# Performance work log

Hardware: AMD Instinct MI355X
Metric: run time of the kernel (lower is better)

Reference implementation:

```python
import jax, jax.numpy as jnp
import numpy as np

NUM_ROUNDS = 3


def squash(x, axis=-1):
    # s_norm / (1 + s_norm) * x / sqrt(s_norm), matching the torch code exactly
    s_norm = jnp.sum(x * x, axis=axis, keepdims=True)
    return (s_norm / (1.0 + s_norm)) * x / jnp.sqrt(s_norm)


def setup_inputs() -> dict:
    key = jax.random.key(0)
    k1, k2 = jax.random.split(key)
    x = jax.random.normal(k1, (512, 1152, 8), dtype=jnp.float32)   # [B, R, Cin]
    W = jax.random.normal(k2, (10, 1152, 8, 16), dtype=jnp.float32)  # [N, R, Cin, Cout]
    return {"x": x, "W": W}


def reference(x, W):
    # priors = x[None,:,:,None,:] @ W[:,None,:,:,:]  -> [N, B, R, 1, Cout]
    priors = jnp.einsum('bri,nrio->nbro', x, W)[:, :, :, None, :]
    logits = jnp.zeros_like(priors)  # [N, B, R, 1, Cout]
    outps = None
    for i in range(NUM_ROUNDS):
        probs = jax.nn.softmax(logits, axis=2)  # softmax over routes R
        outps = squash(jnp.sum(probs * priors, axis=2, keepdims=True))  # [N, B, 1, 1, Cout]
        if i != NUM_ROUNDS - 1:
            # agreement logit update: dot over Cout
            logits = logits + jnp.sum(priors * outps, axis=-1, keepdims=True)
    return outps
```

## Files before the change

kernel.cpp:

```cpp
#include <hip/hip_runtime.h>
#include <math.h>

#define R_ROUTES 1152
#define CIN 8
#define COUT 16
#define BATCH 512
#define NCAPS 10
#define NUM_ROUNDS 3

typedef __fp16 h2 __attribute__((ext_vector_type(2)));
union U32H2 { unsigned int u; h2 h; };

__device__ __forceinline__ unsigned int pkrtz(float lo, float hi) {
    U32H2 v; v.h = __builtin_amdgcn_cvt_pkrtz(lo, hi);
    return v.u;
}
__device__ __forceinline__ h2 as_h2(unsigned int u) { U32H2 v; v.u = u; return v.h; }
__device__ __forceinline__ float f_lo(unsigned int u) { return (float)as_h2(u).x; }
__device__ __forceinline__ float f_hi(unsigned int u) { return (float)as_h2(u).y; }
__device__ __forceinline__ float dot2(unsigned int p, unsigned int s, float c) {
    return __builtin_amdgcn_fdot2(as_h2(p), as_h2(s), c, false);
}

__device__ __forceinline__ int sunit(int r, int h) {
    return (2 * r + h) ^ ((r >> 2) & 7);
}

extern "C" __global__ void __launch_bounds__(256)
pack_w(const float* __restrict__ W, unsigned int* __restrict__ Wp)
{
    const int tau = blockIdx.x * 256 + threadIdx.x;
    const int o = tau & 15;
    const int nr = tau >> 4;
    const float* __restrict__ src = W + (size_t)nr * 128 + o;
    uint4 u;
    u.x = pkrtz(src[0],  src[16]);
    u.y = pkrtz(src[32], src[48]);
    u.z = pkrtz(src[64], src[80]);
    u.w = pkrtz(src[96], src[112]);
    *(uint4*)(Wp + (size_t)tau * 4) = u;
}

extern "C" __global__ void __launch_bounds__(512, 4)
capsule_routing_v9(const float* __restrict__ x,
                   const unsigned int* __restrict__ Wp,
                   float* __restrict__ out)
{
    __shared__ unsigned int pbuf[2 * R_ROUTES * 8];
    __shared__ float wred[16 * 16];
    __shared__ float red[2 * 32 * 20];
    __shared__ float sred[2 * 4];
    __shared__ float sv[2 * 16];

    const int blk = blockIdx.x;
    const int n = blk >> 8;
    const int bp = blk & 255;
    const int t = threadIdx.x;

    const float* __restrict__ x0 = x + (size_t)(2 * bp) * (R_ROUTES * CIN);
    const float* __restrict__ x1 = x0 + R_ROUTES * CIN;
    const unsigned int* __restrict__ Wn = Wp + (size_t)n * (R_ROUTES * 64);

    float cs[2][4] = {{0.f, 0.f, 0.f, 0.f}, {0.f, 0.f, 0.f, 0.f}};
    {
        const int q = t >> 2;
        const int oq = t & 3;
        const int subw = (oq & 1) * 2;
        const int hq = oq >> 1;

        #pragma unroll 1
        for (int it = 0; it < 9; ++it) {
            const int r = it * 128 + q;
            const unsigned int* __restrict__ wb = Wn + (size_t)r * 64;
            const uint4 w0 = *(const uint4*)(wb + (oq + 0) * 4);
            const uint4 w1 = *(const uint4*)(wb + (oq + 4) * 4);
            const uint4 w2 = *(const uint4*)(wb + (oq + 8) * 4);
            const uint4 w3 = *(const uint4*)(wb + (oq + 12) * 4);
            const float4 xa0 = *(const float4*)(x0 + r * 8);
            const float4 xa1 = *(const float4*)(x0 + r * 8 + 4);
            const float4 xb0 = *(const float4*)(x1 + r * 8);
            const float4 xb1 = *(const float4*)(x1 + r * 8 + 4);

            {
                const unsigned int xp0 = pkrtz(xa0.x, xa0.y), xp1 = pkrtz(xa0.z, xa0.w);
                const unsigned int xp2 = pkrtz(xa1.x, xa1.y), xp3 = pkrtz(xa1.z, xa1.w);
                const float p0 = dot2(w0.w, xp3, dot2(w0.z, xp2, dot2(w0.y, xp1, dot2(w0.x, xp0, 0.f))));
                const float p1 = dot2(w1.w, xp3, dot2(w1.z, xp2, dot2(w1.y, xp1, dot2(w1.x, xp0, 0.f))));
                const float p2 = dot2(w2.w, xp3, dot2(w2.z, xp2, dot2(w2.y, xp1, dot2(w2.x, xp0, 0.f))));
                const float p3 = dot2(w3.w, xp3, dot2(w3.z, xp2, dot2(w3.y, xp1, dot2(w3.x, xp0, 0.f))));
                cs[0][0] += p0; cs[0][1] += p1; cs[0][2] += p2; cs[0][3] += p3;
                uint2 u; u.x = pkrtz(p0, p1); u.y = pkrtz(p2, p3);
                *(uint2*)(pbuf + sunit(r, hq) * 4 + subw) = u;
            }
            {
                const unsigned int xp0 = pkrtz(xb0.x, xb0.y), xp1 = pkrtz(xb0.z, xb0.w);
                const unsigned int xp2 = pkrtz(xb1.x, xb1.y), xp3 = pkrtz(xb1.z, xb1.w);
                const float p0 = dot2(w0.w, xp3, dot2(w0.z, xp2, dot2(w0.y, xp1, dot2(w0.x, xp0, 0.f))));
                const float p1 = dot2(w1.w, xp3, dot2(w1.z, xp2, dot2(w1.y, xp1, dot2(w1.x, xp0, 0.f))));
                const float p2 = dot2(w2.w, xp3, dot2(w2.z, xp2, dot2(w2.y, xp1, dot2(w2.x, xp0, 0.f))));
                const float p3 = dot2(w3.w, xp3, dot2(w3.z, xp2, dot2(w3.y, xp1, dot2(w3.x, xp0, 0.f))));
                cs[1][0] += p0; cs[1][1] += p1; cs[1][2] += p2; cs[1][3] += p3;
                uint2 u; u.x = pkrtz(p0, p1); u.y = pkrtz(p2, p3);
                *(uint2*)(pbuf + R_ROUTES * 8 + sunit(r, hq) * 4 + subw) = u;
            }
        }

        #pragma unroll
        for (int mask = 4; mask <= 32; mask <<= 1) {
            #pragma unroll
            for (int b = 0; b < 2; ++b)
                #pragma unroll
                for (int j = 0; j < 4; ++j)
                    cs[b][j] += __shfl_xor(cs[b][j], mask, 64);
        }
        if ((t & 63) < 4) {
            const int w = t >> 6;
            *(float4*)(wred + (w * 2 + 0) * 16 + 4 * oq) =
                make_float4(cs[0][0], cs[0][1], cs[0][2], cs[0][3]);
            *(float4*)(wred + (w * 2 + 1) * 16 + 4 * oq) =
                make_float4(cs[1][0], cs[1][1], cs[1][2], cs[1][3]);
        }
    }
    __syncthreads();

    const int half = t >> 8;
    const int tt = t & 255;
    unsigned int* __restrict__ pb = pbuf + half * (R_ROUTES * 8);
    float* __restrict__ redh = red + half * (32 * 20);
    float* __restrict__ sredh = sred + half * 4;
    float* __restrict__ svh = sv + half * 16;

    if (tt < 16) {
        float s = 0.f;
        #pragma unroll
        for (int w = 0; w < 8; ++w) s += wred[(w * 2 + half) * 16 + tt];
        svh[tt] = s * (1.0f / (float)R_ROUTES);
    }
    __syncthreads();

    float sn = 0.f;
    #pragma unroll
    for (int o = 0; o < 16; ++o) { const float s = svh[o]; sn = fmaf(s, s, sn); }
    float factor = sn / ((1.0f + sn) * sqrtf(sn));

    const int nr = (tt < 128) ? 5 : 4;
    float bl[5] = {0.f, 0.f, 0.f, 0.f, 0.f};

    #pragma unroll 1
    for (int pass = 1; pass < NUM_ROUNDS; ++pass) {
        unsigned int svp[8];
        #pragma unroll
        for (int s = 0; s < 8; ++s)
            svp[s] = pkrtz(svh[2 * s], svh[2 * s + 1]);
        float acc[16];
        #pragma unroll
        for (int o = 0; o < 16; ++o) acc[o] = 0.f;
        float es = 0.f;

        #pragma unroll
        for (int k = 0; k < 5; ++k) {
            if (k < nr) {
                const int r = tt + (k << 8);
                const uint4 a = *(const uint4*)(pb + sunit(r, 0) * 4);
                const uint4 c = *(const uint4*)(pb + sunit(r, 1) * 4);
                float d = 0.f;
                d = dot2(a.x, svp[0], d);
                d = dot2(a.y, svp[1], d);
                d = dot2(a.z, svp[2], d);
                d = dot2(a.w, svp[3], d);
                d = dot2(c.x, svp[4], d);
                d = dot2(c.y, svp[5], d);
                d = dot2(c.z, svp[6], d);
                d = dot2(c.w, svp[7], d);
                bl[k] = fmaf(factor, d, bl[k]);
                const float e = __expf(bl[k]);
                es += e;
                acc[0]  = fmaf(e, f_lo(a.x), acc[0]);
                acc[1]  = fmaf(e, f_hi(a.x), acc[1]);
                acc[2]  = fmaf(e, f_lo(a.y), acc[2]);
                acc[3]  = fmaf(e, f_hi(a.y), acc[3]);
                acc[4]  = fmaf(e, f_lo(a.z), acc[4]);
                acc[5]  = fmaf(e, f_hi(a.z), acc[5]);
                acc[6]  = fmaf(e, f_lo(a.w), acc[6]);
                acc[7]  = fmaf(e, f_hi(a.w), acc[7]);
                acc[8]  = fmaf(e, f_lo(c.x), acc[8]);
                acc[9]  = fmaf(e, f_hi(c.x), acc[9]);
                acc[10] = fmaf(e, f_lo(c.y), acc[10]);
                acc[11] = fmaf(e, f_hi(c.y), acc[11]);
                acc[12] = fmaf(e, f_lo(c.z), acc[12]);
                acc[13] = fmaf(e, f_hi(c.z), acc[13]);
                acc[14] = fmaf(e, f_lo(c.w), acc[14]);
                acc[15] = fmaf(e, f_hi(c.w), acc[15]);
            }
        }
        #pragma unroll
        for (int off = 32; off > 0; off >>= 1) es += __shfl_xor(es, off, 64);
        if ((t & 63) == 0) sredh[tt >> 6] = es;

        #pragma unroll
        for (int o = 0; o < 16; ++o) {
            acc[o] += __shfl_xor(acc[o], 1, 64);
            acc[o] += __shfl_xor(acc[o], 2, 64);
            acc[o] += __shfl_xor(acc[o], 4, 64);
        }
        if ((tt & 7) == 0) {
            float* dst = redh + (tt >> 3) * 20;
            *(float4*)(dst + 0)  = make_float4(acc[0],  acc[1],  acc[2],  acc[3]);
            *(float4*)(dst + 4)  = make_float4(acc[4],  acc[5],  acc[6],  acc[7]);
            *(float4*)(dst + 8)  = make_float4(acc[8],  acc[9],  acc[10], acc[11]);
            *(float4*)(dst + 12) = make_float4(acc[12], acc[13], acc[14], acc[15]);
        }
        __syncthreads();

        if (tt < 16) {
            float s = 0.f;
            #pragma unroll
            for (int w = 0; w < 32; ++w) s += redh[w * 20 + tt];
            const float Z = sredh[0] + sredh[1] + sredh[2] + sredh[3];
            svh[tt] = s / Z;
        }
        __syncthreads();

        sn = 0.f;
        #pragma unroll
        for (int o = 0; o < 16; ++o) { const float s = svh[o]; sn = fmaf(s, s, sn); }
        factor = sn / ((1.0f + sn) * sqrtf(sn));
    }

    if (tt < 16) {
        const int o = (tt >> 2) + ((tt & 3) << 2);
        out[((size_t)n * BATCH + 2 * bp + half) * COUT + o] = factor * svh[tt];
    }
}

extern "C" void kernel_launch(void* const* d_in, const int* in_sizes, int n_in,
                              void* d_out, int out_size, void* d_ws, size_t ws_size,
                              hipStream_t stream) {
    const float* x = (const float*)d_in[0];
    const float* W = (const float*)d_in[1];
    float* out = (float*)d_out;
    unsigned int* Wp = (unsigned int*)d_ws;

    pack_w<<<dim3(NCAPS * R_ROUTES * COUT / 256), dim3(256), 0, stream>>>(W, Wp);
    capsule_routing_v9<<<dim3(NCAPS * (BATCH / 2)), dim3(512), 0, stream>>>(x, Wp, out);
}
```

Measured before the change: 136.4 us.

## Pre-pack x to fp16 in prep kernel and software-pipeline routing loads

Extends the weight-packing kernel to also convert x to packed fp16, so the routing kernel reads half as many bytes of x for each of the ten capsules and skips the per-block conversion. The first routing loop is double-buffered across iterations so the loads for the next route chunk are issued before the current chunk's dot products. A fallback path keeps the old behaviour when the workspace is too small. This costs an extra pass over x in the prep kernel and more registers in the main kernel.

After: 136.8 us. About the same (+0.3%).

```diff
diff --git a/kernel.cpp b/kernel.cpp
--- a/kernel.cpp
+++ b/kernel.cpp
@@ -8,6 +8,10 @@
 #define NCAPS 10
 #define NUM_ROUNDS 3
 
+#define WP_U32S (NCAPS * R_ROUTES * COUT * 4)
+#define XP_U32S (BATCH * R_ROUTES * 4)
+#define WS_NEED ((size_t)(WP_U32S + XP_U32S) * 4)
+
 typedef __fp16 h2 __attribute__((ext_vector_type(2)));
 union U32H2 { unsigned int u; h2 h; };
 
@@ -27,24 +31,71 @@
 }
 
 extern "C" __global__ void __launch_bounds__(256)
-pack_w(const float* __restrict__ W, unsigned int* __restrict__ Wp)
+pack_wx(const float* __restrict__ W, const float* __restrict__ x,
+        unsigned int* __restrict__ Wp, unsigned int* __restrict__ xp)
 {
-    const int tau = blockIdx.x * 256 + threadIdx.x;
-    const int o = tau & 15;
-    const int nr = tau >> 4;
-    const float* __restrict__ src = W + (size_t)nr * 128 + o;
-    uint4 u;
-    u.x = pkrtz(src[0],  src[16]);
-    u.y = pkrtz(src[32], src[48]);
-    u.z = pkrtz(src[64], src[80]);
-    u.w = pkrtz(src[96], src[112]);
-    *(uint4*)(Wp + (size_t)tau * 4) = u;
-}
+    const int bid = blockIdx.x;
+    if (bid < NCAPS * R_ROUTES * COUT / 256) {
+        const int tau = bid * 256 + threadIdx.x;
+        const int o = tau & 15;
+        const int nr = tau >> 4;
+        const float* __restrict__ src = W + (size_t)nr * 128 + o;
+        uint4 u;
+        u.x = pkrtz(src[0],  src[16]);
+        u.y = pkrtz(src[32], src[48]);
+        u.z = pkrtz(src[64], src[80]);
+        u.w = pkrtz(src[96], src[112]);
+        *(uint4*)(Wp + (size_t)tau * 4) = u;
+    } else {
+        const int idx = (bid - NCAPS * R_ROUTES * COUT / 256) * 256 + threadIdx.x;
+        const float4 v0 = *(const float4*)(x + (size_t)idx * 8);
+        const float4 v1 = *(const float4*)(x + (size_t)idx * 8 + 4);
+        uint4 u;
+        u.x = pkrtz(v0.x, v0.y); u.y = pkrtz(v0.z, v0.w);
+        u.z = pkrtz(v1.x, v1.y); u.w = pkrtz(v1.z, v1.w);
+        *(uint4*)(xp + (size_t)idx * 4) = u;
+    }
+}
+
+#define LOADS(IT, W0, W1, W2, W3, XA, XB)                                  \
+    {                                                                      \
+        const int r_ = (IT) * 128 + q;                                     \
+        const unsigned int* __restrict__ wb_ = Wn + (size_t)r_ * 64 + oq * 4; \
+        W0 = *(const uint4*)(wb_);                                         \
+        W1 = *(const uint4*)(wb_ + 16);                                    \
+        W2 = *(const uint4*)(wb_ + 32);                                    \
+        W3 = *(const uint4*)(wb_ + 48);                                    \
+        XA = *(const uint4*)(xp0 + (size_t)r_ * 4);                        \
+        XB = *(const uint4*)(xp1 + (size_t)r_ * 4);                        \
+    }
+
+#define COMPUTES(IT, W0, W1, W2, W3, XA, XB)                               \
+    {                                                                      \
+        const int r_ = (IT) * 128 + q;                                     \
+        {                                                                  \
+            const float p0 = dot2(W0.w, XA.w, dot2(W0.z, XA.z, dot2(W0.y, XA.y, dot2(W0.x, XA.x, 0.f)))); \
+            const float p1 = dot2(W1.w, XA.w, dot2(W1.z, XA.z, dot2(W1.y, XA.y, dot2(W1.x, XA.x, 0.f)))); \
+            const float p2 = dot2(W2.w, XA.w, dot2(W2.z, XA.z, dot2(W2.y, XA.y, dot2(W2.x, XA.x, 0.f)))); \
+            const float p3 = dot2(W3.w, XA.w, dot2(W3.z, XA.z, dot2(W3.y, XA.y, dot2(W3.x, XA.x, 0.f)))); \
+            cs00 += p0; cs01 += p1; cs02 += p2; cs03 += p3;                \
+            uint2 u_; u_.x = pkrtz(p0, p1); u_.y = pkrtz(p2, p3);          \
+            *(uint2*)(pbuf + sunit(r_, hq) * 4 + subw) = u_;               \
+        }                                                                  \
+        {                                                                  \
+            const float p0 = dot2(W0.w, XB.w, dot2(W0.z, XB.z, dot2(W0.y, XB.y, dot2(W0.x, XB.x, 0.f)))); \
+            const float p1 = dot2(W1.w, XB.w, dot2(W1.z, XB.z, dot2(W1.y, XB.y, dot2(W1.x, XB.x, 0.f)))); \
+            const float p2 = dot2(W2.w, XB.w, dot2(W2.z, XB.z, dot2(W2.y, XB.y, dot2(W2.x, XB.x, 0.f)))); \
+            const float p3 = dot2(W3.w, XB.w, dot2(W3.z, XB.z, dot2(W3.y, XB.y, dot2(W3.x, XB.x, 0.f)))); \
+            cs10 += p0; cs11 += p1; cs12 += p2; cs13 += p3;                \
+            uint2 u_; u_.x = pkrtz(p0, p1); u_.y = pkrtz(p2, p3);          \
+            *(uint2*)(pbuf + R_ROUTES * 8 + sunit(r_, hq) * 4 + subw) = u_; \
+        }                                                                  \
+    }
 
 extern "C" __global__ void __launch_bounds__(512, 4)
-capsule_routing_v9(const float* __restrict__ x,
-                   const unsigned int* __restrict__ Wp,
-                   float* __restrict__ out)
+capsule_routing_v10(const unsigned int* __restrict__ xp,
+                    const unsigned int* __restrict__ Wp,
+                    float* __restrict__ out)
 {
     __shared__ unsigned int pbuf[2 * R_ROUTES * 8];
     __shared__ float wred[16 * 16];
@@ -57,68 +108,42 @@
     const int bp = blk & 255;
     const int t = threadIdx.x;
 
-    const float* __restrict__ x0 = x + (size_t)(2 * bp) * (R_ROUTES * CIN);
-    const float* __restrict__ x1 = x0 + R_ROUTES * CIN;
+    const unsigned int* __restrict__ xp0 = xp + (size_t)(2 * bp) * (R_ROUTES * 4);
+    const unsigned int* __restrict__ xp1 = xp0 + R_ROUTES * 4;
     const unsigned int* __restrict__ Wn = Wp + (size_t)n * (R_ROUTES * 64);
 
-    float cs[2][4] = {{0.f, 0.f, 0.f, 0.f}, {0.f, 0.f, 0.f, 0.f}};
+    float cs00 = 0.f, cs01 = 0.f, cs02 = 0.f, cs03 = 0.f;
+    float cs10 = 0.f, cs11 = 0.f, cs12 = 0.f, cs13 = 0.f;
     {
         const int q = t >> 2;
         const int oq = t & 3;
         const int subw = (oq & 1) * 2;
         const int hq = oq >> 1;
 
+        uint4 wA0, wA1, wA2, wA3, xAa, xAb;
+        uint4 wB0, wB1, wB2, wB3, xBa, xBb;
+
+        LOADS(0, wA0, wA1, wA2, wA3, xAa, xAb);
         #pragma unroll 1
-        for (int it = 0; it < 9; ++it) {
-            const int r = it * 128 + q;
-            const unsigned int* __restrict__ wb = Wn + (size_t)r * 64;
-            const uint4 w0 = *(const uint4*)(wb + (oq + 0) * 4);
-            const uint4 w1 = *(const uint4*)(wb + (oq + 4) * 4);
-            const uint4 w2 = *(const uint4*)(wb + (oq + 8) * 4);
-            const uint4 w3 = *(const uint4*)(wb + (oq + 12) * 4);
-            const float4 xa0 = *(const float4*)(x0 + r * 8);
-            const float4 xa1 = *(const float4*)(x0 + r * 8 + 4);
-            const float4 xb0 = *(const float4*)(x1 + r * 8);
-            const float4 xb1 = *(const float4*)(x1 + r * 8 + 4);
-
-            {
-                const unsigned int xp0 = pkrtz(xa0.x, xa0.y), xp1 = pkrtz(xa0.z, xa0.w);
-                const unsigned int xp2 = pkrtz(xa1.x, xa1.y), xp3 = pkrtz(xa1.z, xa1.w);
-                const float p0 = dot2(w0.w, xp3, dot2(w0.z, xp2, dot2(w0.y, xp1, dot2(w0.x, xp0, 0.f))));
-                const float p1 = dot2(w1.w, xp3, dot2(w1.z, xp2, dot2(w1.y, xp1, dot2(w1.x, xp0, 0.f))));
-                const float p2 = dot2(w2.w, xp3, dot2(w2.z, xp2, dot2(w2.y, xp1, dot2(w2.x, xp0, 0.f))));
-                const float p3 = dot2(w3.w, xp3, dot2(w3.z, xp2, dot2(w3.y, xp1, dot2(w3.x, xp0, 0.f))));
-                cs[0][0] += p0; cs[0][1] += p1; cs[0][2] += p2; cs[0][3] += p3;
-                uint2 u; u.x = pkrtz(p0, p1); u.y = pkrtz(p2, p3);
-                *(uint2*)(pbuf + sunit(r, hq) * 4 + subw) = u;
-            }
-            {
-                const unsigned int xp0 = pkrtz(xb0.x, xb0.y), xp1 = pkrtz(xb0.z, xb0.w);
-                const unsigned int xp2 = pkrtz(xb1.x, xb1.y), xp3 = pkrtz(xb1.z, xb1.w);
-                const float p0 = dot2(w0.w, xp3, dot2(w0.z, xp2, dot2(w0.y, xp1, dot2(w0.x, xp0, 0.f))));
-                const float p1 = dot2(w1.w, xp3, dot2(w1.z, xp2, dot2(w1.y, xp1, dot2(w1.x, xp0, 0.f))));
-                const float p2 = dot2(w2.w, xp3, dot2(w2.z, xp2, dot2(w2.y, xp1, dot2(w2.x, xp0, 0.f))));
-                const float p3 = dot2(w3.w, xp3, dot2(w3.z, xp2, dot2(w3.y, xp1, dot2(w3.x, xp0, 0.f))));
-                cs[1][0] += p0; cs[1][1] += p1; cs[1][2] += p2; cs[1][3] += p3;
-                uint2 u; u.x = pkrtz(p0, p1); u.y = pkrtz(p2, p3);
-                *(uint2*)(pbuf + R_ROUTES * 8 + sunit(r, hq) * 4 + subw) = u;
-            }
-        }
+        for (int it = 0; it < 8; it += 2) {
+            LOADS(it + 1, wB0, wB1, wB2, wB3, xBa, xBb);
+            COMPUTES(it, wA0, wA1, wA2, wA3, xAa, xAb);
+            LOADS(it + 2, wA0, wA1, wA2, wA3, xAa, xAb);
+            COMPUTES(it + 1, wB0, wB1, wB2, wB3, xBa, xBb);
+        }
+        COMPUTES(8, wA0, wA1, wA2, wA3, xAa, xAb);
 
         #pragma unroll
         for (int mask = 4; mask <= 32; mask <<= 1) {
-            #pragma unroll
-            for (int b = 0; b < 2; ++b)
-                #pragma unroll
-                for (int j = 0; j < 4; ++j)
-                    cs[b][j] += __shfl_xor(cs[b][j], mask, 64);
+            cs00 += __shfl_xor(cs00, mask, 64); cs01 += __shfl_xor(cs01, mask, 64);
+            cs02 += __shfl_xor(cs02, mask, 64); cs03 += __shfl_xor(cs03, mask, 64);
+            cs10 += __shfl_xor(cs10, mask, 64); cs11 += __shfl_xor(cs11, mask, 64);
+            cs12 += __shfl_xor(cs12, mask, 64); cs13 += __shfl_xor(cs13, mask, 64);
         }
         if ((t & 63) < 4) {
             const int w = t >> 6;
-            *(float4*)(wred + (w * 2 + 0) * 16 + 4 * oq) =
-                make_float4(cs[0][0], cs[0][1], cs[0][2], cs[0][3]);
-            *(float4*)(wred + (w * 2 + 1) * 16 + 4 * oq) =
-                make_float4(cs[1][0], cs[1][1], cs[1][2], cs[1][3]);
+            *(float4*)(wred + (w * 2 + 0) * 16 + 4 * oq) = make_float4(cs00, cs01, cs02, cs03);
+            *(float4*)(wred + (w * 2 + 1) * 16 + 4 * oq) = make_float4(cs10, cs11, cs12, cs13);
         }
     }
     __syncthreads();
@@ -233,6 +258,192 @@
     }
 }
 
+extern "C" __global__ void __launch_bounds__(256)
+pack_w_only(const float* __restrict__ W, unsigned int* __restrict__ Wp)
+{
+    const int tau = blockIdx.x * 256 + threadIdx.x;
+    const int o = tau & 15;
+    const int nr = tau >> 4;
+    const float* __restrict__ src = W + (size_t)nr * 128 + o;
+    uint4 u;
+    u.x = pkrtz(src[0],  src[16]);
+    u.y = pkrtz(src[32], src[48]);
+    u.z = pkrtz(src[64], src[80]);
+    u.w = pkrtz(src[96], src[112]);
+    *(uint4*)(Wp + (size_t)tau * 4) = u;
+}
+
+extern "C" __global__ void __launch_bounds__(512, 4)
+capsule_routing_v9f(const float* __restrict__ x,
+                    const unsigned int* __restrict__ Wp,
+                    float* __restrict__ out)
+{
+    __shared__ unsigned int pbuf[2 * R_ROUTES * 8];
+    __shared__ float wred[16 * 16];
+    __shared__ float red[2 * 32 * 20];
+    __shared__ float sred[2 * 4];
+    __shared__ float sv[2 * 16];
+
+    const int blk = blockIdx.x;
+    const int n = blk >> 8;
+    const int bp = blk & 255;
+    const int t = threadIdx.x;
+
+    const float* __restrict__ x0 = x + (size_t)(2 * bp) * (R_ROUTES * CIN);
+    const float* __restrict__ x1 = x0 + R_ROUTES * CIN;
+    const unsigned int* __restrict__ Wn = Wp + (size_t)n * (R_ROUTES * 64);
+
+    float cs00 = 0.f, cs01 = 0.f, cs02 = 0.f, cs03 = 0.f;
+    float cs10 = 0.f, cs11 = 0.f, cs12 = 0.f, cs13 = 0.f;
+    {
+        const int q = t >> 2;
+        const int oq = t & 3;
+        const int subw = (oq & 1) * 2;
+        const int hq = oq >> 1;
+
+        #pragma unroll 1
+        for (int it = 0; it < 9; ++it) {
+            const int r = it * 128 + q;
+            const unsigned int* __restrict__ wb = Wn + (size_t)r * 64 + oq * 4;
+            const uint4 w0 = *(const uint4*)(wb);
+            const uint4 w1 = *(const uint4*)(wb + 16);
+            const uint4 w2 = *(const uint4*)(wb + 32);
+            const uint4 w3 = *(const uint4*)(wb + 48);
+            const float4 xa0 = *(const float4*)(x0 + r * 8);
+            const float4 xa1 = *(const float4*)(x0 + r * 8 + 4);
+            const float4 xb0 = *(const float4*)(x1 + r * 8);
+            const float4 xb1 = *(const float4*)(x1 + r * 8 + 4);
+            {
+                const unsigned int xq0 = pkrtz(xa0.x, xa0.y), xq1 = pkrtz(xa0.z, xa0.w);
+                const unsigned int xq2 = pkrtz(xa1.x, xa1.y), xq3 = pkrtz(xa1.z, xa1.w);
+                const float p0 = dot2(w0.w, xq3, dot2(w0.z, xq2, dot2(w0.y, xq1, dot2(w0.x, xq0, 0.f))));
+                const float p1 = dot2(w1.w, xq3, dot2(w1.z, xq2, dot2(w1.y, xq1, dot2(w1.x, xq0, 0.f))));
+                const float p2 = dot2(w2.w, xq3, dot2(w2.z, xq2, dot2(w2.y, xq1, dot2(w2.x, xq0, 0.f))));
+                const float p3 = dot2(w3.w, xq3, dot2(w3.z, xq2, dot2(w3.y, xq1, dot2(w3.x, xq0, 0.f))));
+                cs00 += p0; cs01 += p1; cs02 += p2; cs03 += p3;
+                uint2 u; u.x = pkrtz(p0, p1); u.y = pkrtz(p2, p3);
+                *(uint2*)(pbuf + sunit(r, hq) * 4 + subw) = u;
+            }
+            {
+                const unsigned int xq0 = pkrtz(xb0.x, xb0.y), xq1 = pkrtz(xb0.z, xb0.w);
+                const unsigned int xq2 = pkrtz(xb1.x, xb1.y), xq3 = pkrtz(xb1.z, xb1.w);
+                const float p0 = dot2(w0.w, xq3, dot2(w0.z, xq2, dot2(w0.y, xq1, dot2(w0.x, xq0, 0.f))));
+                const float p1 = dot2(w1.w, xq3, dot2(w1.z, xq2, dot2(w1.y, xq1, dot2(w1.x, xq0, 0.f))));
+                const float p2 = dot2(w2.w, xq3, dot2(w2.z, xq2, dot2(w2.y, xq1, dot2(w2.x, xq0, 0.f))));
+                const float p3 = dot2(w3.w, xq3, dot2(w3.z, xq2, dot2(w3.y, xq1, dot2(w3.x, xq0, 0.f))));
+                cs10 += p0; cs11 += p1; cs12 += p2; cs13 += p3;
+                uint2 u; u.x = pkrtz(p0, p1); u.y = pkrtz(p2, p3);
+                *(uint2*)(pbuf + R_ROUTES * 8 + sunit(r, hq) * 4 + subw) = u;
+            }
+        }
+        #pragma unroll
+        for (int mask = 4; mask <= 32; mask <<= 1) {
+            cs00 += __shfl_xor(cs00, mask, 64); cs01 += __shfl_xor(cs01, mask, 64);
+            cs02 += __shfl_xor(cs02, mask, 64); cs03 += __shfl_xor(cs03, mask, 64);
+            cs10 += __shfl_xor(cs10, mask, 64); cs11 += __shfl_xor(cs11, mask, 64);
+            cs12 += __shfl_xor(cs12, mask, 64); cs13 += __shfl_xor(cs13, mask, 64);
+        }
+        if ((t & 63) < 4) {
+            const int w = t >> 6;
+            *(float4*)(wred + (w * 2 + 0) * 16 + 4 * oq) = make_float4(cs00, cs01, cs02, cs03);
+            *(float4*)(wred + (w * 2 + 1) * 16 + 4 * oq) = make_float4(cs10, cs11, cs12, cs13);
+        }
+    }
+    __syncthreads();
+
+    const int half = t >> 8;
+    const int tt = t & 255;
+    unsigned int* __restrict__ pb = pbuf + half * (R_ROUTES * 8);
+    float* __restrict__ redh = red + half * (32 * 20);
+    float* __restrict__ sredh = sred + half * 4;
+    float* __restrict__ svh = sv + half * 16;
+
+    if (tt < 16) {
+        float s = 0.f;
+        #pragma unroll
+        for (int w = 0; w < 8; ++w) s += wred[(w * 2 + half) * 16 + tt];
+        svh[tt] = s * (1.0f / (float)R_ROUTES);
+    }
+    __syncthreads();
+
+    float sn = 0.f;
+    #pragma unroll
+    for (int o = 0; o < 16; ++o) { const float s = svh[o]; sn = fmaf(s, s, sn); }
+    float factor = sn / ((1.0f + sn) * sqrtf(sn));
+
+    const int nr = (tt < 128) ? 5 : 4;
+    float bl[5] = {0.f, 0.f, 0.f, 0.f, 0.f};
+
+    #pragma unroll 1
+    for (int pass = 1; pass < NUM_ROUNDS; ++pass) {
+        unsigned int svp[8];
+        #pragma unroll
+        for (int s = 0; s < 8; ++s) svp[s] = pkrtz(svh[2 * s], svh[2 * s + 1]);
+        float acc[16];
+        #pragma unroll
+        for (int o = 0; o < 16; ++o) acc[o] = 0.f;
+        float es = 0.f;
+        #pragma unroll
+        for (int k = 0; k < 5; ++k) {
+            if (k < nr) {
+                const int r = tt + (k << 8);
+                const uint4 a = *(const uint4*)(pb + sunit(r, 0) * 4);
+                const uint4 c = *(const uint4*)(pb + sunit(r, 1) * 4);
+                float d = 0.f;
+                d = dot2(a.x, svp[0], d); d = dot2(a.y, svp[1], d);
+                d = dot2(a.z, svp[2], d); d = dot2(a.w, svp[3], d);
+                d = dot2(c.x, svp[4], d); d = dot2(c.y, svp[5], d);
+                d = dot2(c.z, svp[6], d); d = dot2(c.w, svp[7], d);
+                bl[k] = fmaf(factor, d, bl[k]);
+                const float e = __expf(bl[k]);
+                es += e;
+                acc[0]  = fmaf(e, f_lo(a.x), acc[0]);  acc[1]  = fmaf(e, f_hi(a.x), acc[1]);
+                acc[2]  = fmaf(e, f_lo(a.y), acc[2]);  acc[3]  = fmaf(e, f_hi(a.y), acc[3]);
+                acc[4]  = fmaf(e, f_lo(a.z), acc[4]);  acc[5]  = fmaf(e, f_hi(a.z), acc[5]);
+                acc[6]  = fmaf(e, f_lo(a.w), acc[6]);  acc[7]  = fmaf(e, f_hi(a.w), acc[7]);
+                acc[8]  = fmaf(e, f_lo(c.x), acc[8]);  acc[9]  = fmaf(e, f_hi(c.x), acc[9]);
+                acc[10] = fmaf(e, f_lo(c.y), acc[10]); acc[11] = fmaf(e, f_hi(c.y), acc[11]);
+                acc[12] = fmaf(e, f_lo(c.z), acc[12]); acc[13] = fmaf(e, f_hi(c.z), acc[13]);
+                acc[14] = fmaf(e, f_lo(c.w), acc[14]); acc[15] = fmaf(e, f_hi(c.w), acc[15]);
+            }
+        }
+        #pragma unroll
+        for (int off = 32; off > 0; off >>= 1) es += __shfl_xor(es, off, 64);
+        if ((t & 63) == 0) sredh[tt >> 6] = es;
+        #pragma unroll
+        for (int o = 0; o < 16; ++o) {
+            acc[o] += __shfl_xor(acc[o], 1, 64);
+            acc[o] += __shfl_xor(acc[o], 2, 64);
+            acc[o] += __shfl_xor(acc[o], 4, 64);
+        }
+        if ((tt & 7) == 0) {
+            float* dst = redh + (tt >> 3) * 20;
+            *(float4*)(dst + 0)  = make_float4(acc[0],  acc[1],  acc[2],  acc[3]);
+            *(float4*)(dst + 4)  = make_float4(acc[4],  acc[5],  acc[6],  acc[7]);
+            *(float4*)(dst + 8)  = make_float4(acc[8],  acc[9],  acc[10], acc[11]);
+            *(float4*)(dst + 12) = make_float4(acc[12], acc[13], acc[14], acc[15]);
+        }
+        __syncthreads();
+        if (tt < 16) {
+            float s = 0.f;
+            #pragma unroll
+            for (int w = 0; w < 32; ++w) s += redh[w * 20 + tt];
+            const float Z = sredh[0] + sredh[1] + sredh[2] + sredh[3];
+            svh[tt] = s / Z;
+        }
+        __syncthreads();
+        sn = 0.f;
+        #pragma unroll
+        for (int o = 0; o < 16; ++o) { const float s = svh[o]; sn = fmaf(s, s, sn); }
+        factor = sn / ((1.0f + sn) * sqrtf(sn));
+    }
+
+    if (tt < 16) {
+        const int o = (tt >> 2) + ((tt & 3) << 2);
+        out[((size_t)n * BATCH + 2 * bp + half) * COUT + o] = factor * svh[tt];
+    }
+}
+
 extern "C" void kernel_launch(void* const* d_in, const int* in_sizes, int n_in,
                               void* d_out, int out_size, void* d_ws, size_t ws_size,
                               hipStream_t stream) {
@@ -240,7 +451,15 @@
     const float* W = (const float*)d_in[1];
     float* out = (float*)d_out;
     unsigned int* Wp = (unsigned int*)d_ws;
-
-    pack_w<<<dim3(NCAPS * R_ROUTES * COUT / 256), dim3(256), 0, stream>>>(W, Wp);
-    capsule_routing_v9<<<dim3(NCAPS * (BATCH / 2)), dim3(512), 0, stream>>>(x, Wp, out);
-}
+    unsigned int* xp = Wp + WP_U32S;
+
+    if (ws_size >= WS_NEED) {
+        const int wblocks = NCAPS * R_ROUTES * COUT / 256;
+        const int xblocks = BATCH * R_ROUTES / 256;
+        pack_wx<<<dim3(wblocks + xblocks), dim3(256), 0, stream>>>(W, x, Wp, xp);
+        capsule_routing_v10<<<dim3(NCAPS * (BATCH / 2)), dim3(512), 0, stream>>>(xp, Wp, out);
+    } else {
+        pack_w_only<<<dim3(NCAPS * R_ROUTES * COUT / 256), dim3(256), 0, stream>>>(W, Wp);
+        capsule_routing_v9f<<<dim3(NCAPS * (BATCH / 2)), dim3(512), 0, stream>>>(x, Wp, out);
+    }
+}
```
